# Kernel tuning notes

Measured on AMD Instinct MI355X. Metric: run time of the kernel, lower is better.

Reference implementation:

```python
import jax, jax.numpy as jnp
import numpy as np

N_NODES = 100000
N_EDGES = 1600000
IN_F = 64
HIDDEN = 128
HIDDEN2 = HIDDEN // 2
N_CLASSES = 10


def setup_inputs() -> dict:
    key = jax.random.key(0)
    ks = jax.random.split(key, 8)
    x = jax.random.normal(ks[0], (N_NODES, IN_F), dtype=jnp.float32)
    edge_index = jax.random.randint(ks[1], (2, N_EDGES), 0, N_NODES, dtype=jnp.int64 if jax.config.jax_enable_x64 else jnp.int32)
    # Linear params (PyTorch nn.Linear: y = x @ W.T + b); store as [in, out] for einsum-free matmul
    def lin(k, fi, fo):
        bound = 1.0 / np.sqrt(fi)
        kw, kb = jax.random.split(k)
        W = jax.random.uniform(kw, (fi, fo), minval=-bound, maxval=bound, dtype=jnp.float32)
        b = jax.random.uniform(kb, (fo,), minval=-bound, maxval=bound, dtype=jnp.float32)
        return W, b
    W1, b1 = lin(ks[2], IN_F, HIDDEN)
    W2, b2 = lin(ks[3], HIDDEN, HIDDEN2)
    W3, b3 = lin(ks[4], HIDDEN2, N_CLASSES)
    return {"x": x, "edge_index": edge_index, "n_nodes": N_NODES,
            "W1": W1, "b1": b1, "W2": W2, "b2": b2, "W3": W3, "b3": b3}


def gcn_layer(x, row, col, n_nodes, W, b):
    # gather source features, scatter-add into destination nodes
    agg = jax.ops.segment_sum(x[row], col, num_segments=n_nodes)  # [N, F]
    deg = jax.ops.segment_sum(jnp.ones_like(col, dtype=x.dtype), col, num_segments=n_nodes)
    deg = jnp.maximum(deg, 1.0)
    return (agg / deg[:, None]) @ W + b


def reference(x, edge_index, n_nodes, W1, b1, W2, b2, W3, b3):
    row, col = edge_index[0], edge_index[1]
    h = jax.nn.relu(gcn_layer(x, row, col, n_nodes, W1, b1))
    # dropout is identity in eval mode
    h = jax.nn.relu(gcn_layer(h, row, col, n_nodes, W2, b2))
    return h @ W3 + b3
```

## Files before the change

### kernel.cpp

```cpp
#include <hip/hip_runtime.h>

#define N_NODES 100000
#define N_EDGES 1600000
#define IN_F 64
#define HID 128
#define HID2 64
#define NCLS 10

#define SEG 64

#define NBUCK 256
#define SUBR 391
#define CAP2 7000
#define EBA 6250

typedef __attribute__((ext_vector_type(8))) short bfrag;
typedef __attribute__((ext_vector_type(4))) float f32x4;

__device__ __forceinline__ unsigned short bf_rne(float f) {
  unsigned int u = __float_as_uint(f);
  u += 0x7fffu + ((u >> 16) & 1u);
  return (unsigned short)(u >> 16);
}

__global__ __launch_bounds__(256) void cast_k(const float* __restrict__ x,
                                              unsigned short* __restrict__ xb) {
  int i = blockIdx.x * blockDim.x + threadIdx.x;
  const float4* xf4 = (const float4*)x;
  float4 a = xf4[2 * i];
  float4 b = xf4[2 * i + 1];
  ushort4 o0, o1;
  o0.x = bf_rne(a.x); o0.y = bf_rne(a.y); o0.z = bf_rne(a.z); o0.w = bf_rne(a.w);
  o1.x = bf_rne(b.x); o1.y = bf_rne(b.y); o1.z = bf_rne(b.z); o1.w = bf_rne(b.w);
  ushort4* ob = (ushort4*)xb;
  ob[2 * i] = o0;
  ob[2 * i + 1] = o1;
}

__global__ __launch_bounds__(256) void wtrans_k(const float* __restrict__ W1,
                                                const float* __restrict__ W2,
                                                unsigned short* __restrict__ W1t,
                                                unsigned short* __restrict__ W2t,
                                                int* __restrict__ bcnt) {
  int i = blockIdx.x * 256 + threadIdx.x;
  if (blockIdx.x == 0) bcnt[threadIdx.x] = 0;
  if (i < IN_F * HID) {
    int j = i >> 6, k = i & 63;
    W1t[i] = bf_rne(W1[k * HID + j]);
  } else {
    int i2 = i - IN_F * HID;
    int j = i2 >> 7, k = i2 & 127;
    W2t[i2] = bf_rne(W2[k * HID2 + j]);
  }
}

__global__ __launch_bounds__(256) void binA_k(const int* __restrict__ row,
                                              const int* __restrict__ col,
                                              int* __restrict__ bcnt,
                                              unsigned int* __restrict__ pairs) {
  __shared__ int hcnt[NBUCK];
  __shared__ int hbase[NBUCK];
  int t = threadIdx.x;
  hcnt[t] = 0;
  __syncthreads();
  int e0 = blockIdx.x * EBA;
  int e1 = e0 + EBA;
  for (int e = e0 + t; e < e1; e += 256) {
    int b = col[e] / SUBR;
    atomicAdd(&hcnt[b], 1);
  }
  __syncthreads();
  hbase[t] = atomicAdd(&bcnt[t], hcnt[t]);
  hcnt[t] = 0;
  __syncthreads();
  for (int e = e0 + t; e < e1; e += 256) {
    int dst = col[e];
    int src = row[e];
    int b = dst / SUBR;
    int pos = hbase[b] + atomicAdd(&hcnt[b], 1);
    pairs[(size_t)b * CAP2 + pos] =
        ((unsigned)(dst - b * SUBR) << 17) | (unsigned)src;
  }
}

__global__ __launch_bounds__(512) void binB_k(const unsigned int* __restrict__ pairs,
                                              const int* __restrict__ bcnt,
                                              int* __restrict__ cursors,
                                              int* __restrict__ csr_src) {
  __shared__ int cur[SUBR];
  int b = blockIdx.x;
  int t = threadIdx.x;
  int lo = b * SUBR;
  for (int i = t; i < SUBR; i += 512) cur[i] = 0;
  __syncthreads();
  int cnt = bcnt[b];
  const unsigned int* bp = pairs + (size_t)b * CAP2;
  for (int i = t; i < cnt; i += 512) {
    unsigned w = bp[i];
    int local = w >> 17;
    int src = (int)(w & 0x1ffffu);
    int pos = atomicAdd(&cur[local], 1);
    if (pos < SEG) csr_src[(size_t)(lo + local) * SEG + pos] = src;
  }
  __syncthreads();
  for (int i = t; i < SUBR; i += 512) {
    int n = lo + i;
    if (n < N_NODES) {
      int d = cur[i];
      if (d > SEG) d = SEG;
      cursors[n] = n * SEG + d;
      int cons = d <= 32 ? 32 : ((d + 15) & ~15);
      for (int q = d; q < cons; q++) csr_src[(size_t)n * SEG + q] = 0;
    }
  }
}

__device__ __forceinline__ float4 gather_node(const uint2* __restrict__ vb,
                                              const int4* __restrict__ csr4,
                                              int n, int d, int eg, int fc,
                                              float zx, float zy, float zz,
                                              float zw) {
  float ax = 0.f, ay = 0.f, az = 0.f, aw = 0.f;
  int s4 = n * 16;
  int4 ia = csr4[s4 + eg];
  int4 ib = csr4[s4 + 4 + eg];
  uint2 r0 = vb[(size_t)(unsigned)ia.x * 16 + fc];
  uint2 r1 = vb[(size_t)(unsigned)ia.y * 16 + fc];
  uint2 r2 = vb[(size_t)(unsigned)ia.z * 16 + fc];
  uint2 r3 = vb[(size_t)(unsigned)ia.w * 16 + fc];
  uint2 r4 = vb[(size_t)(unsigned)ib.x * 16 + fc];
  uint2 r5 = vb[(size_t)(unsigned)ib.y * 16 + fc];
  uint2 r6 = vb[(size_t)(unsigned)ib.z * 16 + fc];
  uint2 r7 = vb[(size_t)(unsigned)ib.w * 16 + fc];
#define ACC1(r)                                                     \
  {                                                                 \
    ax += __uint_as_float((r).x << 16);                             \
    ay += __uint_as_float((r).x & 0xffff0000u);                     \
    az += __uint_as_float((r).y << 16);                             \
    aw += __uint_as_float((r).y & 0xffff0000u);                     \
  }
  ACC1(r0) ACC1(r1) ACC1(r2) ACC1(r3) ACC1(r4) ACC1(r5) ACC1(r6) ACC1(r7)
  int cons = 32;
  if (d > 32) {
    cons = (d + 15) & ~15;
    for (int p = n * SEG + 32; p < n * SEG + cons; p += 16) {
      int4 it = csr4[(p >> 2) + eg];
      uint2 t0 = vb[(size_t)(unsigned)it.x * 16 + fc];
      uint2 t1 = vb[(size_t)(unsigned)it.y * 16 + fc];
      uint2 t2 = vb[(size_t)(unsigned)it.z * 16 + fc];
      uint2 t3 = vb[(size_t)(unsigned)it.w * 16 + fc];
      ACC1(t0) ACC1(t1) ACC1(t2) ACC1(t3)
    }
  }
#undef ACC1
  ax += __shfl_xor(ax, 16); ay += __shfl_xor(ay, 16);
  az += __shfl_xor(az, 16); aw += __shfl_xor(aw, 16);
  ax += __shfl_xor(ax, 32); ay += __shfl_xor(ay, 32);
  az += __shfl_xor(az, 32); aw += __shfl_xor(aw, 32);
  float pc = (float)(cons - d);
  return make_float4(ax - pc * zx, ay - pc * zy, az - pc * zz, aw - pc * zw);
}

__global__ __launch_bounds__(256) void gather1_k(
    const unsigned short* __restrict__ xb, const int* __restrict__ cursors,
    const int* __restrict__ csr_src, unsigned short* __restrict__ xm) {
  int t = threadIdx.x;
  int lane = t & 63;
  int eg = lane >> 4;
  int fc = lane & 15;
  int n0 = (blockIdx.x * 4 + (t >> 6)) * 4;
  const uint2* vb = (const uint2*)xb;
  const int4* csr4 = (const int4*)csr_src;
  uint2 z = vb[fc];
  float zx = __uint_as_float(z.x << 16);
  float zy = __uint_as_float(z.x & 0xffff0000u);
  float zz = __uint_as_float(z.y << 16);
  float zw = __uint_as_float(z.y & 0xffff0000u);
  for (int i = 0; i < 4; i++) {
    int n = n0 + i;
    int d = cursors[n] - n * SEG;
    float4 a = gather_node(vb, csr4, n, d, eg, fc, zx, zy, zz, zw);
    if (eg == 0) {
      float inv = 1.0f / (d < 1 ? 1.0f : (float)d);
      ushort4 o;
      o.x = bf_rne(a.x * inv); o.y = bf_rne(a.y * inv);
      o.z = bf_rne(a.z * inv); o.w = bf_rne(a.w * inv);
      *(ushort4*)&xm[(size_t)n * IN_F + fc * 4] = o;
    }
  }
}

__global__ __launch_bounds__(256) void gather2_k(
    const unsigned short* __restrict__ g, const int* __restrict__ cursors,
    const int* __restrict__ csr_src, const float* __restrict__ b2,
    unsigned short* __restrict__ hm) {
  int t = threadIdx.x;
  int lane = t & 63;
  int eg = lane >> 4;
  int fc = lane & 15;
  int n0 = (blockIdx.x * 4 + (t >> 6)) * 4;
  const uint2* vb = (const uint2*)g;
  const int4* csr4 = (const int4*)csr_src;
  uint2 z = vb[fc];
  float zx = __uint_as_float(z.x << 16);
  float zy = __uint_as_float(z.x & 0xffff0000u);
  float zz = __uint_as_float(z.y << 16);
  float zw = __uint_as_float(z.y & 0xffff0000u);
  const float4* b2f4 = (const float4*)b2;
  float4 bb = b2f4[fc];
  for (int i = 0; i < 4; i++) {
    int n = n0 + i;
    int d = cursors[n] - n * SEG;
    float4 a = gather_node(vb, csr4, n, d, eg, fc, zx, zy, zz, zw);
    if (eg == 0) {
      float inv = 1.0f / (d < 1 ? 1.0f : (float)d);
      float vx = a.x * inv + bb.x;
      float vy = a.y * inv + bb.y;
      float vz = a.z * inv + bb.z;
      float vw = a.w * inv + bb.w;
      ushort4 o;
      o.x = bf_rne(vx > 0.0f ? vx : 0.0f);
      o.y = bf_rne(vy > 0.0f ? vy : 0.0f);
      o.z = bf_rne(vz > 0.0f ? vz : 0.0f);
      o.w = bf_rne(vw > 0.0f ? vw : 0.0f);
      *(ushort4*)&hm[(size_t)n * HID2 + fc * 4] = o;
    }
  }
}

#define NB1 32
#define XS_S 72
#define HS_S 136
__global__ __launch_bounds__(512) void mm12_k(
    const unsigned short* __restrict__ xm, const unsigned short* __restrict__ W1t,
    const float* __restrict__ b1, const unsigned short* __restrict__ W2t,
    unsigned short* __restrict__ g) {
  __shared__ unsigned short xsb[NB1 * XS_S];
  __shared__ unsigned short hsb[NB1 * HS_S];
  int t = threadIdx.x;
  int node0 = blockIdx.x * NB1;
  {
    int r = t >> 4, u = t & 15;
    *(ushort4*)&xsb[r * XS_S + u * 4] =
        ((const ushort4*)xm)[(size_t)(node0 + r) * (IN_F / 4) + u];
  }
  __syncthreads();
  int wave = t >> 6;
  int lane = t & 63;
  int lr = lane & 15;
  int kb = lane >> 4;
  {
    int col = wave * 16 + lr;
    bfrag wf0 = *(const bfrag*)&W1t[col * IN_F + kb * 8];
    bfrag wf1 = *(const bfrag*)&W1t[col * IN_F + 32 + kb * 8];
    float bb = b1[col];
#pragma unroll
    for (int m = 0; m < 2; m++) {
      f32x4 acc = {0.f, 0.f, 0.f, 0.f};
      bfrag a0 = *(const bfrag*)&xsb[(m * 16 + lr) * XS_S + kb * 8];
      bfrag a1 = *(const bfrag*)&xsb[(m * 16 + lr) * XS_S + 32 + kb * 8];
      acc = __builtin_amdgcn_mfma_f32_16x16x32_bf16(a0, wf0, acc, 0, 0, 0);
      acc = __builtin_amdgcn_mfma_f32_16x16x32_bf16(a1, wf1, acc, 0, 0, 0);
#pragma unroll
      for (int q = 0; q < 4; q++) {
        int r = m * 16 + kb * 4 + q;
        float v = acc[q] + bb;
        hsb[r * HS_S + col] = bf_rne(v > 0.0f ? v : 0.0f);
      }
    }
  }
  __syncthreads();
  {
    int m = wave >> 2;
    int col = (wave & 3) * 16 + lr;
    f32x4 acc = {0.f, 0.f, 0.f, 0.f};
#pragma unroll
    for (int s = 0; s < 4; s++) {
      bfrag af = *(const bfrag*)&hsb[(m * 16 + lr) * HS_S + s * 32 + kb * 8];
      bfrag bf = *(const bfrag*)&W2t[col * HID + s * 32 + kb * 8];
      acc = __builtin_amdgcn_mfma_f32_16x16x32_bf16(af, bf, acc, 0, 0, 0);
    }
#pragma unroll
    for (int q = 0; q < 4; q++) {
      int r = m * 16 + kb * 4 + q;
      g[(size_t)(node0 + r) * HID2 + col] = bf_rne(acc[q]);
    }
  }
}

#define NBH3 25
__global__ __launch_bounds__(256) void head_k(
    const unsigned short* __restrict__ hm, const float* __restrict__ W3,
    const float* __restrict__ b3, float* __restrict__ out) {
  __shared__ float W3l[HID2 * NCLS];
  __shared__ float hsl[NBH3][HID2 + 4];
  int t = threadIdx.x;
  for (int i = t; i < HID2 * NCLS; i += 256) W3l[i] = W3[i];
  int node0 = blockIdx.x * NBH3;
  for (int u = t; u < NBH3 * (HID2 / 4); u += 256) {
    int r = u >> 4, c = u & 15;
    ushort4 v = ((const ushort4*)hm)[(size_t)(node0 + r) * (HID2 / 4) + c];
    hsl[r][c * 4 + 0] = __uint_as_float((unsigned)v.x << 16);
    hsl[r][c * 4 + 1] = __uint_as_float((unsigned)v.y << 16);
    hsl[r][c * 4 + 2] = __uint_as_float((unsigned)v.z << 16);
    hsl[r][c * 4 + 3] = __uint_as_float((unsigned)v.w << 16);
  }
  __syncthreads();
  if (t < NBH3 * NCLS) {
    int n = t / NCLS;
    int c = t - n * NCLS;
    float a = b3[c];
    for (int k = 0; k < HID2; k++) a += hsl[n][k] * W3l[k * NCLS + c];
    out[(size_t)(node0 + n) * NCLS + c] = a;
  }
}

extern "C" void kernel_launch(void* const* d_in, const int* in_sizes, int n_in,
                              void* d_out, int out_size, void* d_ws, size_t ws_size,
                              hipStream_t stream) {
  const float* x  = (const float*)d_in[0];
  const int*   ei = (const int*)d_in[1];
  const int*   row = ei;
  const int*   col = ei + N_EDGES;
  const float* W1 = (const float*)d_in[3];
  const float* b1 = (const float*)d_in[4];
  const float* W2 = (const float*)d_in[5];
  const float* b2 = (const float*)d_in[6];
  const float* W3 = (const float*)d_in[7];
  const float* b3 = (const float*)d_in[8];
  float* out = (float*)d_out;

  char* ws = (char*)d_ws;
  int*            cursors = (int*)ws;
  int*            bcnt    = (int*)(ws + (512 << 10));
  unsigned short* W1t     = (unsigned short*)(ws + (520 << 10));
  unsigned short* W2t     = (unsigned short*)(ws + (552 << 10));
  int*            csr_src = (int*)(ws + (1 << 20));
  unsigned int*   pairs   = (unsigned int*)(ws + (28 << 20));
  unsigned short* xb      = (unsigned short*)(ws + (36 << 20));
  unsigned short* g       = (unsigned short*)(ws + (49 << 20));
  unsigned short* xm      = (unsigned short*)(ws + (62 << 20));
  unsigned short* hm      = xm;

  wtrans_k<<<(IN_F * HID + HID * HID2) / 256, 256, 0, stream>>>(W1, W2, W1t, W2t, bcnt);
  cast_k<<<N_NODES * IN_F / 8 / 256, 256, 0, stream>>>(x, xb);
  binA_k<<<N_EDGES / EBA, 256, 0, stream>>>(row, col, bcnt, pairs);
  binB_k<<<NBUCK, 512, 0, stream>>>(pairs, bcnt, cursors, csr_src);

  gather1_k<<<N_NODES / 16, 256, 0, stream>>>(xb, cursors, csr_src, xm);
  mm12_k<<<N_NODES / NB1, 512, 0, stream>>>(xm, W1t, b1, W2t, g);

  gather2_k<<<N_NODES / 16, 256, 0, stream>>>(g, cursors, csr_src, b2, hm);
  head_k<<<N_NODES / NBH3, 256, 0, stream>>>(hm, W3, b3, out);
}
```

Before: 153.8 us.

## Slice-sort CSR neighbors by source range and pad with dedicated zero row

binB now counts each destination's edges per source slice (8 slices of 12500 nodes) and places them grouped by slice, padding each slice group to a multiple of 4 so that every int4 index load hits one source region. This should improve cache locality of the feature gathers. Padding entries now point to a dedicated zero row at index N_NODES instead of node 0, which removes the correction subtraction in the gather. The gather loop is unified to iterate T/16 chunks with no fixed 32-entry minimum. The cost is an extra counting pass in binB, more padding slots, and a larger SEG of 96 that grows the CSR buffer.

```diff
diff --git a/kernel.cpp b/kernel.cpp
--- a/kernel.cpp
+++ b/kernel.cpp
@@ -7,12 +7,17 @@
 #define HID2 64
 #define NCLS 10
 
-#define SEG 64
+#define SEG 96
+#define SEGI4 (SEG / 4)
+#define NSLICE 8
+#define SLICE 12500
 
 #define NBUCK 256
 #define SUBR 391
 #define CAP2 7000
 #define EBA 6250
+
+#define ZROW N_NODES
 
 typedef __attribute__((ext_vector_type(8))) short bfrag;
 typedef __attribute__((ext_vector_type(4))) float f32x4;
@@ -35,6 +40,13 @@
   ushort4* ob = (ushort4*)xb;
   ob[2 * i] = o0;
   ob[2 * i + 1] = o1;
+}
+
+__global__ void zr_k(unsigned short* __restrict__ xb,
+                     unsigned short* __restrict__ g) {
+  int t = threadIdx.x;
+  xb[(size_t)ZROW * IN_F + t] = 0;
+  g[(size_t)ZROW * HID2 + t] = 0;
 }
 
 __global__ __launch_bounds__(256) void wtrans_k(const float* __restrict__ W1,
@@ -85,53 +97,69 @@
 
 __global__ __launch_bounds__(512) void binB_k(const unsigned int* __restrict__ pairs,
                                               const int* __restrict__ bcnt,
-                                              int* __restrict__ cursors,
+                                              int* __restrict__ meta,
                                               int* __restrict__ csr_src) {
-  __shared__ int cur[SUBR];
+  __shared__ int cnt[SUBR][NSLICE];
+  __shared__ int cur[SUBR][NSLICE];
   int b = blockIdx.x;
   int t = threadIdx.x;
   int lo = b * SUBR;
-  for (int i = t; i < SUBR; i += 512) cur[i] = 0;
-  __syncthreads();
-  int cnt = bcnt[b];
+  for (int i = t; i < SUBR * NSLICE; i += 512) ((int*)cnt)[i] = 0;
+  __syncthreads();
+  int cntB = bcnt[b];
   const unsigned int* bp = pairs + (size_t)b * CAP2;
-  for (int i = t; i < cnt; i += 512) {
+  for (int i = t; i < cntB; i += 512) {
     unsigned w = bp[i];
     int local = w >> 17;
     int src = (int)(w & 0x1ffffu);
-    int pos = atomicAdd(&cur[local], 1);
+    atomicAdd(&cnt[local][src / SLICE], 1);
+  }
+  __syncthreads();
+  for (int n = t; n < SUBR; n += 512) {
+    int gn = lo + n;
+    if (gn >= N_NODES) continue;
+    int c[NSLICE];
+    int d = 0, Tp = 0;
+    for (int p = 0; p < NSLICE; p++) {
+      c[p] = cnt[n][p];
+      d += c[p];
+      Tp += (c[p] + 3) & ~3;
+    }
+    int T;
+    int s = 0;
+    if (Tp <= SEG) {
+      for (int p = 0; p < NSLICE; p++) {
+        cur[n][p] = s;
+        s += (c[p] + 3) & ~3;
+      }
+      T = (Tp + 15) & ~15;
+    } else {
+      for (int p = 0; p < NSLICE; p++) {
+        cur[n][p] = s;
+        s += c[p];
+      }
+      int dc = d > SEG ? SEG : d;
+      T = (dc + 15) & ~15;
+    }
+    meta[gn] = d | (T << 16);
+    int base = gn * SEG;
+    for (int q = 0; q < T; q++) csr_src[base + q] = ZROW;
+  }
+  __syncthreads();
+  for (int i = t; i < cntB; i += 512) {
+    unsigned w = bp[i];
+    int local = w >> 17;
+    int src = (int)(w & 0x1ffffu);
+    int pos = atomicAdd(&cur[local][src / SLICE], 1);
     if (pos < SEG) csr_src[(size_t)(lo + local) * SEG + pos] = src;
-  }
-  __syncthreads();
-  for (int i = t; i < SUBR; i += 512) {
-    int n = lo + i;
-    if (n < N_NODES) {
-      int d = cur[i];
-      if (d > SEG) d = SEG;
-      cursors[n] = n * SEG + d;
-      int cons = d <= 32 ? 32 : ((d + 15) & ~15);
-      for (int q = d; q < cons; q++) csr_src[(size_t)n * SEG + q] = 0;
-    }
   }
 }
 
 __device__ __forceinline__ float4 gather_node(const uint2* __restrict__ vb,
                                               const int4* __restrict__ csr4,
-                                              int n, int d, int eg, int fc,
-                                              float zx, float zy, float zz,
-                                              float zw) {
+                                              int n, int T, int eg, int fc) {
   float ax = 0.f, ay = 0.f, az = 0.f, aw = 0.f;
-  int s4 = n * 16;
-  int4 ia = csr4[s4 + eg];
-  int4 ib = csr4[s4 + 4 + eg];
-  uint2 r0 = vb[(size_t)(unsigned)ia.x * 16 + fc];
-  uint2 r1 = vb[(size_t)(unsigned)ia.y * 16 + fc];
-  uint2 r2 = vb[(size_t)(unsigned)ia.z * 16 + fc];
-  uint2 r3 = vb[(size_t)(unsigned)ia.w * 16 + fc];
-  uint2 r4 = vb[(size_t)(unsigned)ib.x * 16 + fc];
-  uint2 r5 = vb[(size_t)(unsigned)ib.y * 16 + fc];
-  uint2 r6 = vb[(size_t)(unsigned)ib.z * 16 + fc];
-  uint2 r7 = vb[(size_t)(unsigned)ib.w * 16 + fc];
+  int b4 = n * SEGI4;
 #define ACC1(r)                                                     \
   {                                                                 \
     ax += __uint_as_float((r).x << 16);                             \
@@ -139,30 +167,24 @@
     az += __uint_as_float((r).y << 16);                             \
     aw += __uint_as_float((r).y & 0xffff0000u);                     \
   }
-  ACC1(r0) ACC1(r1) ACC1(r2) ACC1(r3) ACC1(r4) ACC1(r5) ACC1(r6) ACC1(r7)
-  int cons = 32;
-  if (d > 32) {
-    cons = (d + 15) & ~15;
-    for (int p = n * SEG + 32; p < n * SEG + cons; p += 16) {
-      int4 it = csr4[(p >> 2) + eg];
-      uint2 t0 = vb[(size_t)(unsigned)it.x * 16 + fc];
-      uint2 t1 = vb[(size_t)(unsigned)it.y * 16 + fc];
-      uint2 t2 = vb[(size_t)(unsigned)it.z * 16 + fc];
-      uint2 t3 = vb[(size_t)(unsigned)it.w * 16 + fc];
-      ACC1(t0) ACC1(t1) ACC1(t2) ACC1(t3)
-    }
+  for (int c = 0; c < T; c += 16) {
+    int4 iu = csr4[b4 + (c >> 2) + eg];
+    uint2 r0 = vb[(size_t)(unsigned)iu.x * 16 + fc];
+    uint2 r1 = vb[(size_t)(unsigned)iu.y * 16 + fc];
+    uint2 r2 = vb[(size_t)(unsigned)iu.z * 16 + fc];
+    uint2 r3 = vb[(size_t)(unsigned)iu.w * 16 + fc];
+    ACC1(r0) ACC1(r1) ACC1(r2) ACC1(r3)
   }
 #undef ACC1
   ax += __shfl_xor(ax, 16); ay += __shfl_xor(ay, 16);
   az += __shfl_xor(az, 16); aw += __shfl_xor(aw, 16);
   ax += __shfl_xor(ax, 32); ay += __shfl_xor(ay, 32);
   az += __shfl_xor(az, 32); aw += __shfl_xor(aw, 32);
-  float pc = (float)(cons - d);
-  return make_float4(ax - pc * zx, ay - pc * zy, az - pc * zz, aw - pc * zw);
+  return make_float4(ax, ay, az, aw);
 }
 
 __global__ __launch_bounds__(256) void gather1_k(
-    const unsigned short* __restrict__ xb, const int* __restrict__ cursors,
+    const unsigned short* __restrict__ xb, const int* __restrict__ meta,
     const int* __restrict__ csr_src, unsigned short* __restrict__ xm) {
   int t = threadIdx.x;
   int lane = t & 63;
@@ -171,15 +193,12 @@
   int n0 = (blockIdx.x * 4 + (t >> 6)) * 4;
   const uint2* vb = (const uint2*)xb;
   const int4* csr4 = (const int4*)csr_src;
-  uint2 z = vb[fc];
-  float zx = __uint_as_float(z.x << 16);
-  float zy = __uint_as_float(z.x & 0xffff0000u);
-  float zz = __uint_as_float(z.y << 16);
-  float zw = __uint_as_float(z.y & 0xffff0000u);
   for (int i = 0; i < 4; i++) {
     int n = n0 + i;
-    int d = cursors[n] - n * SEG;
-    float4 a = gather_node(vb, csr4, n, d, eg, fc, zx, zy, zz, zw);
+    int m = meta[n];
+    int d = m & 0xffff;
+    int T = m >> 16;
+    float4 a = gather_node(vb, csr4, n, T, eg, fc);
     if (eg == 0) {
       float inv = 1.0f / (d < 1 ? 1.0f : (float)d);
       ushort4 o;
@@ -191,7 +210,7 @@
 }
 
 __global__ __launch_bounds__(256) void gather2_k(
-    const unsigned short* __restrict__ g, const int* __restrict__ cursors,
+    const unsigned short* __restrict__ g, const int* __restrict__ meta,
     const int* __restrict__ csr_src, const float* __restrict__ b2,
     unsigned short* __restrict__ hm) {
   int t = threadIdx.x;
@@ -201,17 +220,14 @@
   int n0 = (blockIdx.x * 4 + (t >> 6)) * 4;
   const uint2* vb = (const uint2*)g;
   const int4* csr4 = (const int4*)csr_src;
-  uint2 z = vb[fc];
-  float zx = __uint_as_float(z.x << 16);
-  float zy = __uint_as_float(z.x & 0xffff0000u);
-  float zz = __uint_as_float(z.y << 16);
-  float zw = __uint_as_float(z.y & 0xffff0000u);
   const float4* b2f4 = (const float4*)b2;
   float4 bb = b2f4[fc];
   for (int i = 0; i < 4; i++) {
     int n = n0 + i;
-    int d = cursors[n] - n * SEG;
-    float4 a = gather_node(vb, csr4, n, d, eg, fc, zx, zy, zz, zw);
+    int m = meta[n];
+    int d = m & 0xffff;
+    int T = m >> 16;
+    float4 a = gather_node(vb, csr4, n, T, eg, fc);
     if (eg == 0) {
       float inv = 1.0f / (d < 1 ? 1.0f : (float)d);
       float vx = a.x * inv + bb.x;
@@ -331,25 +347,26 @@
   float* out = (float*)d_out;
 
   char* ws = (char*)d_ws;
-  int*            cursors = (int*)ws;
+  int*            meta    = (int*)ws;
   int*            bcnt    = (int*)(ws + (512 << 10));
   unsigned short* W1t     = (unsigned short*)(ws + (520 << 10));
   unsigned short* W2t     = (unsigned short*)(ws + (552 << 10));
   int*            csr_src = (int*)(ws + (1 << 20));
-  unsigned int*   pairs   = (unsigned int*)(ws + (28 << 20));
-  unsigned short* xb      = (unsigned short*)(ws + (36 << 20));
-  unsigned short* g       = (unsigned short*)(ws + (49 << 20));
-  unsigned short* xm      = (unsigned short*)(ws + (62 << 20));
+  unsigned int*   pairs   = (unsigned int*)(ws + (40 << 20));
+  unsigned short* xb      = (unsigned short*)(ws + (48 << 20));
+  unsigned short* g       = (unsigned short*)(ws + (62 << 20));
+  unsigned short* xm      = (unsigned short*)(ws + (76 << 20));
   unsigned short* hm      = xm;
 
   wtrans_k<<<(IN_F * HID + HID * HID2) / 256, 256, 0, stream>>>(W1, W2, W1t, W2t, bcnt);
   cast_k<<<N_NODES * IN_F / 8 / 256, 256, 0, stream>>>(x, xb);
+  zr_k<<<1, 64, 0, stream>>>(xb, g);
   binA_k<<<N_EDGES / EBA, 256, 0, stream>>>(row, col, bcnt, pairs);
-  binB_k<<<NBUCK, 512, 0, stream>>>(pairs, bcnt, cursors, csr_src);
-
-  gather1_k<<<N_NODES / 16, 256, 0, stream>>>(xb, cursors, csr_src, xm);
+  binB_k<<<NBUCK, 512, 0, stream>>>(pairs, bcnt, meta, csr_src);
+
+  gather1_k<<<N_NODES / 16, 256, 0, stream>>>(xb, meta, csr_src, xm);
   mm12_k<<<N_NODES / NB1, 512, 0, stream>>>(xm, W1t, b1, W2t, g);
 
-  gather2_k<<<N_NODES / 16, 256, 0, stream>>>(g, cursors, csr_src, b2, hm);
+  gather2_k<<<N_NODES / 16, 256, 0, stream>>>(g, meta, csr_src, b2, hm);
   head_k<<<N_NODES / NBH3, 256, 0, stream>>>(hm, W3, b3, out);
 }
```

Result: slower. 178.0 us (+15.7%).
